# Optimization experiments

Measured on AMD Instinct MI355X. Metric: run time of the kernel, lower is better.

## Reference

```python
import jax, jax.numpy as jnp
import numpy as np

B, S, D = 2, 2048, 4096
NH, NKV = 32, 8
HD = D // NH  # 128
N_REP = NH // NKV  # 4


def setup_inputs() -> dict:
    key = jax.random.key(0)
    ks = jax.random.split(key, 5)
    scale = 0.02
    return {
        "x": jax.random.normal(ks[0], (B, S, D), dtype=jnp.float32),
        "wq": jax.random.normal(ks[1], (D, NH * HD), dtype=jnp.float32) * scale,
        "wk": jax.random.normal(ks[2], (D, NKV * HD), dtype=jnp.float32) * scale,
        "wv": jax.random.normal(ks[3], (D, NKV * HD), dtype=jnp.float32) * scale,
        "wo": jax.random.normal(ks[4], (NH * HD, D), dtype=jnp.float32) * scale,
    }


def reference(x, wq, wk, wv, wo):
    bsz, toks, _ = x.shape
    q = (x @ wq).reshape(bsz, toks, NH, HD)      # [B,S,NH,HD]
    k = (x @ wk).reshape(bsz, toks, NKV, HD)     # [B,S,NKV,HD]
    v = (x @ wv).reshape(bsz, toks, NKV, HD)
    # GQA: fold n_rep into einsum instead of materializing repeated K/V.
    qg = q.reshape(bsz, toks, NKV, N_REP, HD)    # group query heads per kv head
    scores = jnp.einsum('bqgrd,bkgd->bgrqk', qg, k) / jnp.sqrt(jnp.asarray(HD, x.dtype))
    attn = jax.nn.softmax(scores.astype(jnp.float32), axis=-1).astype(x.dtype)
    out = jnp.einsum('bgrqk,bkgd->bqgrd', attn, v)  # [B,S,NKV,N_REP,HD]
    out = out.reshape(bsz, toks, NH * HD)
    return out @ wo
```

## Files before the change

kernel.cpp:

```cpp
#include <hip/hip_runtime.h>
#include <math.h>

typedef _Float16 f16;
using f16x8 = __attribute__((ext_vector_type(8))) _Float16;
using f32x4 = __attribute__((ext_vector_type(4))) float;

#define BATCH 2
#define SEQ   2048
#define DMODEL 4096
#define NH    32
#define NKV   8
#define HD    128
#define MTOK  (BATCH*SEQ)

__global__ __launch_bounds__(256) void cvt_f32_f16_k(const float* __restrict__ in,
                                                     f16* __restrict__ out, int n8) {
  int i = blockIdx.x * 256 + threadIdx.x;
  if (i >= n8) return;
  const float4* p = reinterpret_cast<const float4*>(in) + (size_t)i * 2;
  float4 a = p[0], b = p[1];
  f16x8 o = { (f16)a.x, (f16)a.y, (f16)a.z, (f16)a.w,
              (f16)b.x, (f16)b.y, (f16)b.z, (f16)b.w };
  reinterpret_cast<f16x8*>(out)[i] = o;
}

__global__ __launch_bounds__(256) void transpose_cvt_k(const float* __restrict__ w,
                                                       f16* __restrict__ wt, int Kd, int Nd,
                                                       float scale) {
  __shared__ float tile[32][33];
  const int t = threadIdx.x;
  const int n0 = blockIdx.x * 32, k0 = blockIdx.y * 32;
  const int r = t >> 3, c4 = (t & 7) << 2;
  const float4 v = *reinterpret_cast<const float4*>(w + (size_t)(k0 + r) * Nd + n0 + c4);
  tile[r][c4 + 0] = v.x; tile[r][c4 + 1] = v.y; tile[r][c4 + 2] = v.z; tile[r][c4 + 3] = v.w;
  __syncthreads();
  union { f16 h[4]; ushort4 u4; } pk;
  pk.h[0] = (f16)(tile[c4 + 0][r] * scale);
  pk.h[1] = (f16)(tile[c4 + 1][r] * scale);
  pk.h[2] = (f16)(tile[c4 + 2][r] * scale);
  pk.h[3] = (f16)(tile[c4 + 3][r] * scale);
  *reinterpret_cast<ushort4*>(wt + (size_t)(n0 + r) * Kd + k0 + c4) = pk.u4;
}

template<int MODE>
__global__ __launch_bounds__(256) void gemm_bt_k(const f16* __restrict__ A,
                                                 const f16* __restrict__ BT,
                                                 void* __restrict__ Cv,
                                                 int M, int N, int K) {
  __shared__ f16 Alds[128 * 64];
  __shared__ f16 Blds[128 * 64];
  const int t = threadIdx.x, lane = t & 63, w = t >> 6;
  const int nbn = N >> 7;
  const int nwg = gridDim.x;
  const int cpx = nwg >> 3;
  const int bid = blockIdx.x;
  const int swz = (bid & 7) * cpx + (bid >> 3);
  const int bm = swz / nbn, bn = swz % nbn;
  const size_t m0 = (size_t)bm << 7, n0 = (size_t)bn << 7;

  const int srow = t >> 3;
  const int sslot = t & 7;
  char* ldsAw = (char*)Alds + w * 1024;
  char* ldsBw = (char*)Blds + w * 1024;

  f32x4 acc[4][4];
#pragma unroll
  for (int i = 0; i < 4; i++)
#pragma unroll
    for (int j = 0; j < 4; j++) acc[i][j] = f32x4{0.f, 0.f, 0.f, 0.f};

  const int wr = (w >> 1) << 6, wc = (w & 1) << 6;
  const int ll = lane & 15, lg = lane >> 4;

  for (int kt = 0; kt < K; kt += 64) {
    __syncthreads();
#pragma unroll
    for (int p = 0; p < 4; p++) {
      const int row = srow + (p << 5);
      const int ssrc = (sslot ^ (row & 7)) << 3;
      const f16* gA = A + (m0 + row) * (size_t)K + kt + ssrc;
      __builtin_amdgcn_global_load_lds((const __attribute__((address_space(1))) void*)gA,
          (__attribute__((address_space(3))) void*)(ldsAw + p * 4096), 16, 0, 0);
      const f16* gB = BT + (n0 + row) * (size_t)K + kt + ssrc;
      __builtin_amdgcn_global_load_lds((const __attribute__((address_space(1))) void*)gB,
          (__attribute__((address_space(3))) void*)(ldsBw + p * 4096), 16, 0, 0);
    }
    __syncthreads();
#pragma unroll
    for (int kk = 0; kk < 2; kk++) {
      f16x8 af[4], bfr[4];
      const int slot = (kk << 2) + lg;
#pragma unroll
      for (int i = 0; i < 4; i++) {
        const int r = wr + (i << 4) + ll;
        af[i] = *reinterpret_cast<const f16x8*>((const char*)Alds + r * 128 + ((slot ^ (r & 7)) << 4));
      }
#pragma unroll
      for (int j = 0; j < 4; j++) {
        const int r = wc + (j << 4) + ll;
        bfr[j] = *reinterpret_cast<const f16x8*>((const char*)Blds + r * 128 + ((slot ^ (r & 7)) << 4));
      }
#pragma unroll
      for (int i = 0; i < 4; i++)
#pragma unroll
        for (int j = 0; j < 4; j++)
          acc[i][j] = __builtin_amdgcn_mfma_f32_16x16x32_f16(af[i], bfr[j], acc[i][j], 0, 0, 0);
    }
  }

#pragma unroll
  for (int i = 0; i < 4; i++) {
    const size_t mrow = m0 + wr + (i << 4) + (lg << 2);
#pragma unroll
    for (int j = 0; j < 4; j++) {
      const size_t ncol = n0 + wc + (j << 4) + ll;
      if (MODE == 0) {
        f16* C = (f16*)Cv;
#pragma unroll
        for (int r = 0; r < 4; r++) C[(mrow + r) * N + ncol] = (f16)acc[i][j][r];
      } else if (MODE == 2) {
        float* C = (float*)Cv;
#pragma unroll
        for (int r = 0; r < 4; r++) C[(mrow + r) * N + ncol] = acc[i][j][r];
      } else if (MODE == 3) {
        f16* Kc = (f16*)Cv;
        f16* Vt = (f16*)Cv + (size_t)MTOK * NKV * HD;
        if ((int)ncol < 1024) {
#pragma unroll
          for (int r = 0; r < 4; r++) Kc[(mrow + r) * 1024 + ncol] = (f16)acc[i][j][r];
        } else {
          const int nc = (int)ncol - 1024;
          const int kvh = nc >> 7, d = nc & 127;
          const int b = (int)(mrow >> 11), sc = (int)(mrow & 2047);
          union { f16 h[4]; ushort4 u4; } pk;
#pragma unroll
          for (int r = 0; r < 4; r++) pk.h[r] = (f16)acc[i][j][r];
          *reinterpret_cast<ushort4*>(Vt + (((size_t)(b * NKV + kvh) * HD + d) * SEQ + sc)) = pk.u4;
        }
      }
    }
  }
}

template<int MODE>
__global__ __launch_bounds__(512, 2) void gemm256_k(const f16* __restrict__ A,
                                                    const f16* __restrict__ BT,
                                                    void* __restrict__ Cv,
                                                    int M, int N, int K) {
  __shared__ f16 lds[2 * 4 * 128 * 64];
  char* ldsb = (char*)lds;

  const int t = threadIdx.x, lane = t & 63, w = t >> 6;
  const int wm = w >> 2, wn = w & 3;
  const int ll = lane & 15, lg = lane >> 4;
  const int nbn = N >> 8;
  const int nwg = gridDim.x, cpx = nwg >> 3, bid = blockIdx.x;
  const int swz = (bid & 7) * cpx + (bid >> 3);
  const int bm = swz / nbn, bn = swz % nbn;
  const size_t m0 = (size_t)bm << 8, n0 = (size_t)bn << 8;
  const int NT = K >> 6;

  auto stage = [&](int bufI, int unit, int ktS) {
    const f16* base = (unit < 2) ? (A + (m0 + (size_t)(unit & 1) * 128) * (size_t)K)
                                 : (BT + (n0 + (size_t)(unit & 1) * 128) * (size_t)K);
#pragma unroll
    for (int rr = 0; rr < 2; rr++) {
      const int u = t + rr * 512;
      const int row = u >> 3, lin = u & 7;
      const int slot = lin ^ (row & 7);
      const f16* src = base + (size_t)row * K + ktS + slot * 8;
      char* dst = ldsb + (size_t)(bufI * 4 + unit) * 16384 + (size_t)(w * 64 + rr * 512) * 16;
      __builtin_amdgcn_global_load_lds((const __attribute__((address_space(1))) void*)src,
          (__attribute__((address_space(3))) void*)dst, 16, 0, 0);
    }
  };

  f32x4 acc[8][4];
#pragma unroll
  for (int i = 0; i < 8; i++)
#pragma unroll
    for (int j = 0; j < 4; j++) acc[i][j] = f32x4{0.f, 0.f, 0.f, 0.f};

  f16x8 af[4][2];
  f16x8 bfr[2][2][2];

  stage(0, 0, 0); stage(0, 2, 0); stage(0, 3, 0); stage(0, 1, 0);
  stage(1, 0, 64); stage(1, 2, 64); stage(1, 3, 64);
  asm volatile("s_waitcnt vmcnt(6)" ::: "memory");
  __builtin_amdgcn_sched_barrier(0);
  __builtin_amdgcn_s_barrier();

#define PH(RBUF, RDA, RDB, SBUF, SUNIT, STILE, VM, MH, NHQ) do {                          \
    if ((RDA) >= 0) {                                                                     \
      const char* ab = ldsb + (size_t)((RBUF) * 4 + (RDA)) * 16384;                       \
      _Pragma("unroll") for (int mi = 0; mi < 4; mi++)                                    \
        _Pragma("unroll") for (int kk = 0; kk < 2; kk++)                                  \
          af[mi][kk] = *reinterpret_cast<const f16x8*>(ab + (mi * 32 + wm * 16 + ll) * 128\
                               + ((((kk << 2) + lg) ^ (ll & 7)) << 4));                   \
    }                                                                                     \
    if ((RDB) >= 0) {                                                                     \
      const char* bb = ldsb + (size_t)((RBUF) * 4 + 2 + (RDB)) * 16384;                   \
      _Pragma("unroll") for (int ni = 0; ni < 2; ni++)                                    \
        _Pragma("unroll") for (int kk = 0; kk < 2; kk++)                                  \
          bfr[RDB][ni][kk] = *reinterpret_cast<const f16x8*>(bb +                         \
                               (wn * 32 + ni * 16 + ll) * 128                             \
                               + ((((kk << 2) + lg) ^ (ll & 7)) << 4));                   \
    }                                                                                     \
    stage((SBUF), (SUNIT), ((STILE) & (NT - 1)) << 6);                                    \
    if (VM) { asm volatile("s_waitcnt vmcnt(6)" ::: "memory");                            \
              __builtin_amdgcn_sched_barrier(0); }                                        \
    __builtin_amdgcn_s_barrier();                                                         \
    asm volatile("s_waitcnt lgkmcnt(0)" ::: "memory");                                    \
    __builtin_amdgcn_sched_barrier(0);                                                    \
    __builtin_amdgcn_s_setprio(1);                                                        \
    _Pragma("unroll") for (int kk = 0; kk < 2; kk++)                                      \
      _Pragma("unroll") for (int mi = 0; mi < 4; mi++)                                    \
        _Pragma("unroll") for (int ni = 0; ni < 2; ni++)                                  \
          acc[(MH) * 4 + mi][(NHQ) * 2 + ni] = __builtin_amdgcn_mfma_f32_16x16x32_f16(    \
              af[mi][kk], bfr[NHQ][ni][kk], acc[(MH) * 4 + mi][(NHQ) * 2 + ni], 0, 0, 0); \
    __builtin_amdgcn_s_setprio(0);                                                        \
    __builtin_amdgcn_s_barrier();                                                         \
  } while (0)

  for (int tt = 0; tt < NT; tt += 2) {
    PH(0,  0,  0, 1, 1, tt + 1, false, 0, 0);
    PH(0, -1,  1, 0, 0, tt + 2, false, 0, 1);
    PH(0,  1, -1, 0, 2, tt + 2, false, 1, 0);
    PH(0, -1, -1, 0, 3, tt + 2, true , 1, 1);
    PH(1,  0,  0, 0, 1, tt + 2, false, 0, 0);
    PH(1, -1,  1, 1, 0, tt + 3, false, 0, 1);
    PH(1,  1, -1, 1, 2, tt + 3, false, 1, 0);
    PH(1, -1, -1, 1, 3, tt + 3, true , 1, 1);
  }
#undef PH

#pragma unroll
  for (int mh = 0; mh < 2; mh++)
#pragma unroll
    for (int mi = 0; mi < 4; mi++) {
      const size_t r0 = m0 + mh * 128 + mi * 32 + wm * 16 + lg * 4;
#pragma unroll
      for (int nh = 0; nh < 2; nh++)
#pragma unroll
        for (int ni = 0; ni < 2; ni++) {
          const size_t c = n0 + nh * 128 + wn * 32 + ni * 16 + ll;
          const f32x4 v = acc[mh * 4 + mi][nh * 2 + ni];
          if (MODE == 0) {
            f16* C = (f16*)Cv;
#pragma unroll
            for (int rr = 0; rr < 4; rr++) C[(r0 + rr) * N + c] = (f16)v[rr];
          } else {
            float* C = (float*)Cv;
#pragma unroll
            for (int rr = 0; rr < 4; rr++) C[(r0 + rr) * N + c] = v[rr];
          }
        }
    }
}

__global__ __launch_bounds__(512) void attn_k7(const f16* __restrict__ Q,
                                               const f16* __restrict__ Kb,
                                               const f16* __restrict__ VT,
                                               f16* __restrict__ ctx) {
  __shared__ f16 Klds[2][64 * 128];
  __shared__ f16 Vlds[2][128 * 64];
  __shared__ f16 Plds[8][16 * 64];

  const int t = threadIdx.x, lane = t & 63, w = t >> 6;
  const int bid = blockIdx.x;
  const int swz = (bid & 7) * 128 + (bid >> 3);
  const int qt = swz & 63, kvh = (swz >> 6) & 7, b = swz >> 9;
  const int h = kvh * 4 + (w & 3);
  const int q0 = qt * 32 + (w >> 2) * 16;
  const int ll = lane & 15, lg = lane >> 4;

  const f16* Qb = Q + ((size_t)(b * SEQ + q0) * NH + h) * HD;
  const f16* Kh = Kb + ((size_t)b * SEQ * NKV + kvh) * HD;
  const f16* Vh = VT + ((size_t)(b * NKV + kvh)) * HD * SEQ;

  f16x8 qf[4];
#pragma unroll
  for (int kd = 0; kd < 4; kd++)
    qf[kd] = *reinterpret_cast<const f16x8*>(Qb + (size_t)ll * (NH * HD) + kd * 32 + lg * 8);

  float m_ = -INFINITY;
  float l_ = 0.f;
  f32x4 o[8];
#pragma unroll
  for (int df = 0; df < 8; df++) o[df] = f32x4{0.f, 0.f, 0.f, 0.f};

  const float THR = 11.5416f;

  auto stage = [&](int bufi, int kt) {
#pragma unroll
    for (int rr = 0; rr < 2; rr++) {
      const int u = w * 128 + rr * 64 + lane;
      const int krow = u >> 4, klin = u & 15;
      const int kslot = klin ^ (krow & 7);
      const f16* ksrc = Kh + (size_t)(kt + krow) * (NKV * HD) + kslot * 8;
      __builtin_amdgcn_global_load_lds((const __attribute__((address_space(1))) void*)ksrc,
          (__attribute__((address_space(3))) void*)((char*)&Klds[bufi][0] + (size_t)u * 16), 16, 0, 0);
      const int vrow = u >> 3, vlin = u & 7;
      const int vslot = vlin ^ (vrow & 7);
      const f16* vsrc = Vh + (size_t)vrow * SEQ + kt + vslot * 8;
      __builtin_amdgcn_global_load_lds((const __attribute__((address_space(1))) void*)vsrc,
          (__attribute__((address_space(3))) void*)((char*)&Vlds[bufi][0] + (size_t)u * 16), 16, 0, 0);
    }
  };

  stage(0, 0);
  __syncthreads();

  for (int kt = 0; kt < SEQ; kt += 64) {
    const int buf = (kt >> 6) & 1;
    if (kt + 64 < SEQ) stage(buf ^ 1, kt + 64);

    const char* Kt = (const char*)Klds[buf];
    const char* Vt = (const char*)Vlds[buf];

    f32x4 s[4];
#pragma unroll
    for (int nf = 0; nf < 4; nf++) {
      f32x4 a = f32x4{0.f, 0.f, 0.f, 0.f};
#pragma unroll
      for (int kd = 0; kd < 4; kd++) {
        const int row = nf * 16 + ll;
        f16x8 kf = *reinterpret_cast<const f16x8*>(
            Kt + row * 256 + ((((kd << 2) + lg) ^ (row & 7)) << 4));
        a = __builtin_amdgcn_mfma_f32_16x16x32_f16(kf, qf[kd], a, 0, 0, 0);
      }
      s[nf] = a;
    }

    float mx = s[0][0];
#pragma unroll
    for (int nf = 0; nf < 4; nf++)
#pragma unroll
      for (int r = 0; r < 4; r++) mx = fmaxf(mx, s[nf][r]);

    if (!__all((int)(mx <= m_ + THR))) {
      float mr = fmaxf(mx, __shfl_xor(mx, 16, 64));
      mr = fmaxf(mr, __shfl_xor(mr, 32, 64));
      const float mn = fmaxf(m_, mr);
      const float corrq = __builtin_amdgcn_exp2f(m_ - mn);
      m_ = mn;
      l_ *= corrq;
#pragma unroll
      for (int r = 0; r < 4; r++) {
        const float c = __shfl(corrq, (lane & 48) | (lg * 4 + r), 64);
#pragma unroll
        for (int df = 0; df < 8; df++) o[df][r] *= c;
      }
    }

    float rs = 0.f;
#pragma unroll
    for (int nf = 0; nf < 4; nf++)
#pragma unroll
      for (int r = 0; r < 4; r++) {
        const float p = __builtin_amdgcn_exp2f(s[nf][r] - m_);
        s[nf][r] = p;
        rs += p;
      }
    rs += __shfl_xor(rs, 16, 64);
    rs += __shfl_xor(rs, 32, 64);
    l_ += rs;

    char* Pw = (char*)&Plds[w][0];
#pragma unroll
    for (int nf = 0; nf < 4; nf++) {
      union { f16 h[4]; ushort4 u4; } pk;
#pragma unroll
      for (int r = 0; r < 4; r++) pk.h[r] = (f16)s[nf][r];
      *reinterpret_cast<ushort4*>(Pw + ll * 128 + ((nf * 32 + lg * 8) ^ ((ll & 7) << 4))) = pk.u4;
    }

    f16x8 pf[2];
#pragma unroll
    for (int kf = 0; kf < 2; kf++)
      pf[kf] = *reinterpret_cast<const f16x8*>(Pw + ll * 128 + (((kf << 6) + (lg << 4)) ^ ((ll & 7) << 4)));

#pragma unroll
    for (int kf = 0; kf < 2; kf++)
#pragma unroll
      for (int df = 0; df < 8; df++) {
        const int row = df * 16 + ll;
        f16x8 vf = *reinterpret_cast<const f16x8*>(
            Vt + row * 128 + ((((kf << 2) + lg) ^ (row & 7)) << 4));
        o[df] = __builtin_amdgcn_mfma_f32_16x16x32_f16(pf[kf], vf, o[df], 0, 0, 0);
      }

    __syncthreads();
  }

  float inv[4];
#pragma unroll
  for (int r = 0; r < 4; r++) {
    const float lq = __shfl(l_, (lane & 48) | (lg * 4 + r), 64);
    inv[r] = 1.0f / lq;
  }
  f16* cb = ctx + ((size_t)(b * SEQ + q0) * NH + h) * HD;
#pragma unroll
  for (int df = 0; df < 8; df++)
#pragma unroll
    for (int r = 0; r < 4; r++)
      cb[(size_t)(lg * 4 + r) * (NH * HD) + df * 16 + ll] = (f16)(o[df][r] * inv[r]);
}

extern "C" void kernel_launch(void* const* d_in, const int* in_sizes, int n_in,
                              void* d_out, int out_size, void* d_ws, size_t ws_size,
                              hipStream_t stream) {
  (void)in_sizes; (void)n_in; (void)out_size;
  const float* x  = (const float*)d_in[0];
  const float* wq = (const float*)d_in[1];
  const float* wk = (const float*)d_in[2];
  const float* wv = (const float*)d_in[3];
  const float* wo = (const float*)d_in[4];
  float* out = (float*)d_out;

  const size_t SZ_X  = (size_t)MTOK * DMODEL * sizeof(f16);
  const size_t SZ_KV = (size_t)MTOK * NKV * HD * sizeof(f16);
  if (ws_size < 3 * SZ_X + 2 * SZ_KV) return;

  char* ws = (char*)d_ws;
  f16* xh  = (f16*)ws;
  f16* wT  = (f16*)(ws + SZ_X);
  f16* Qb  = (f16*)(ws + 2 * SZ_X);
  f16* Kb  = (f16*)(ws + 3 * SZ_X);
  f16* VTb = (f16*)(ws + 3 * SZ_X + SZ_KV);

  const float KSC2 = 0.08838834764831845f * 1.4426950408889634f;

  cvt_f32_f16_k<<<dim3(MTOK * DMODEL / 8 / 256), 256, 0, stream>>>(x, xh, MTOK * DMODEL / 8);

  transpose_cvt_k<<<dim3(DMODEL / 32, DMODEL / 32), 256, 0, stream>>>(wq, wT, DMODEL, DMODEL, KSC2);
  gemm256_k<0><<<dim3((MTOK / 256) * (DMODEL / 256)), 512, 0, stream>>>(xh, wT, Qb, MTOK, DMODEL, DMODEL);

  transpose_cvt_k<<<dim3(NKV * HD / 32, DMODEL / 32), 256, 0, stream>>>(wk, wT, DMODEL, NKV * HD, 1.0f);
  transpose_cvt_k<<<dim3(NKV * HD / 32, DMODEL / 32), 256, 0, stream>>>(wv, wT + (size_t)1024 * DMODEL, DMODEL, NKV * HD, 1.0f);
  gemm_bt_k<3><<<dim3((MTOK / 128) * (2048 / 128)), 256, 0, stream>>>(xh, wT, Kb, MTOK, 2048, DMODEL);

  attn_k7<<<dim3(BATCH * NKV * (SEQ / 32)), 512, 0, stream>>>(Qb, Kb, VTb, xh);

  transpose_cvt_k<<<dim3(DMODEL / 32, DMODEL / 32), 256, 0, stream>>>(wo, wT, DMODEL, DMODEL, 1.0f);
  gemm256_k<2><<<dim3((MTOK / 256) * (DMODEL / 256)), 512, 0, stream>>>(xh, wT, out, MTOK, DMODEL, DMODEL);
}
```

Measured before the change: 551.4 us.

## Process two 16-row query tiles per wave in attention and merge K/V weight transposes

The attention kernel now has each wave handle 32 query rows, as two 16-row halves, against each staged K/V tile. This doubles the reuse of every K and V tile loaded into LDS and halves the number of workgroups and global K/V loads. In exchange each wave holds twice as many accumulator and Q registers, and the launch bound asks for 2 blocks per CU, which risks register pressure or spills. The two separate wk/wv transpose launches are also merged into one launch that uses a z grid dimension.

```diff
diff --git a/kernel.cpp b/kernel.cpp
--- a/kernel.cpp
+++ b/kernel.cpp
@@ -40,6 +40,26 @@
   pk.h[2] = (f16)(tile[c4 + 2][r] * scale);
   pk.h[3] = (f16)(tile[c4 + 3][r] * scale);
   *reinterpret_cast<ushort4*>(wt + (size_t)(n0 + r) * Kd + k0 + c4) = pk.u4;
+}
+
+__global__ __launch_bounds__(256) void transpose_cvt2_k(const float* __restrict__ w0,
+                                                        const float* __restrict__ w1,
+                                                        f16* __restrict__ wt, int Kd, int Nd) {
+  __shared__ float tile[32][33];
+  const float* w = blockIdx.z ? w1 : w0;
+  f16* dst = wt + (size_t)blockIdx.z * Nd * Kd;
+  const int t = threadIdx.x;
+  const int n0 = blockIdx.x * 32, k0 = blockIdx.y * 32;
+  const int r = t >> 3, c4 = (t & 7) << 2;
+  const float4 v = *reinterpret_cast<const float4*>(w + (size_t)(k0 + r) * Nd + n0 + c4);
+  tile[r][c4 + 0] = v.x; tile[r][c4 + 1] = v.y; tile[r][c4 + 2] = v.z; tile[r][c4 + 3] = v.w;
+  __syncthreads();
+  union { f16 h[4]; ushort4 u4; } pk;
+  pk.h[0] = (f16)tile[c4 + 0][r];
+  pk.h[1] = (f16)tile[c4 + 1][r];
+  pk.h[2] = (f16)tile[c4 + 2][r];
+  pk.h[3] = (f16)tile[c4 + 3][r];
+  *reinterpret_cast<ushort4*>(dst + (size_t)(n0 + r) * Kd + k0 + c4) = pk.u4;
 }
 
 template<int MODE>
@@ -258,36 +278,37 @@
     }
 }
 
-__global__ __launch_bounds__(512) void attn_k7(const f16* __restrict__ Q,
-                                               const f16* __restrict__ Kb,
-                                               const f16* __restrict__ VT,
-                                               f16* __restrict__ ctx) {
+__global__ __launch_bounds__(512, 2) void attn_k8(const f16* __restrict__ Q,
+                                                  const f16* __restrict__ Kb,
+                                                  const f16* __restrict__ VT,
+                                                  f16* __restrict__ ctx) {
   __shared__ f16 Klds[2][64 * 128];
   __shared__ f16 Vlds[2][128 * 64];
   __shared__ f16 Plds[8][16 * 64];
 
   const int t = threadIdx.x, lane = t & 63, w = t >> 6;
   const int bid = blockIdx.x;
-  const int swz = (bid & 7) * 128 + (bid >> 3);
-  const int qt = swz & 63, kvh = (swz >> 6) & 7, b = swz >> 9;
+  const int swz = (bid & 7) * 64 + (bid >> 3);
+  const int qt = swz & 31, kvh = (swz >> 5) & 7, b = swz >> 8;
   const int h = kvh * 4 + (w & 3);
-  const int q0 = qt * 32 + (w >> 2) * 16;
+  const int q0 = qt * 64 + (w >> 2) * 32;
   const int ll = lane & 15, lg = lane >> 4;
 
   const f16* Qb = Q + ((size_t)(b * SEQ + q0) * NH + h) * HD;
   const f16* Kh = Kb + ((size_t)b * SEQ * NKV + kvh) * HD;
   const f16* Vh = VT + ((size_t)(b * NKV + kvh)) * HD * SEQ;
 
-  f16x8 qf[4];
-#pragma unroll
-  for (int kd = 0; kd < 4; kd++)
-    qf[kd] = *reinterpret_cast<const f16x8*>(Qb + (size_t)ll * (NH * HD) + kd * 32 + lg * 8);
-
-  float m_ = -INFINITY;
-  float l_ = 0.f;
-  f32x4 o[8];
-#pragma unroll
-  for (int df = 0; df < 8; df++) o[df] = f32x4{0.f, 0.f, 0.f, 0.f};
+  f16x8 qf0[4], qf1[4];
+#pragma unroll
+  for (int kd = 0; kd < 4; kd++) {
+    qf0[kd] = *reinterpret_cast<const f16x8*>(Qb + (size_t)ll * (NH * HD) + kd * 32 + lg * 8);
+    qf1[kd] = *reinterpret_cast<const f16x8*>(Qb + (size_t)(16 + ll) * (NH * HD) + kd * 32 + lg * 8);
+  }
+
+  float m0_ = -INFINITY, l0_ = 0.f, m1_ = -INFINITY, l1_ = 0.f;
+  f32x4 o0[8], o1[8];
+#pragma unroll
+  for (int df = 0; df < 8; df++) { o0[df] = f32x4{0.f, 0.f, 0.f, 0.f}; o1[df] = f32x4{0.f, 0.f, 0.f, 0.f}; }
 
   const float THR = 11.5416f;
 
@@ -308,16 +329,7 @@
     }
   };
 
-  stage(0, 0);
-  __syncthreads();
-
-  for (int kt = 0; kt < SEQ; kt += 64) {
-    const int buf = (kt >> 6) & 1;
-    if (kt + 64 < SEQ) stage(buf ^ 1, kt + 64);
-
-    const char* Kt = (const char*)Klds[buf];
-    const char* Vt = (const char*)Vlds[buf];
-
+  auto half = [&](const char* Kt, const f16x8* qf, float& m_, float& l_, f32x4* o, f16x8* pf) {
     f32x4 s[4];
 #pragma unroll
     for (int nf = 0; nf < 4; nf++) {
@@ -374,11 +386,24 @@
       for (int r = 0; r < 4; r++) pk.h[r] = (f16)s[nf][r];
       *reinterpret_cast<ushort4*>(Pw + ll * 128 + ((nf * 32 + lg * 8) ^ ((ll & 7) << 4))) = pk.u4;
     }
-
-    f16x8 pf[2];
 #pragma unroll
     for (int kf = 0; kf < 2; kf++)
       pf[kf] = *reinterpret_cast<const f16x8*>(Pw + ll * 128 + (((kf << 6) + (lg << 4)) ^ ((ll & 7) << 4)));
+  };
+
+  stage(0, 0);
+  __syncthreads();
+
+  for (int kt = 0; kt < SEQ; kt += 64) {
+    const int buf = (kt >> 6) & 1;
+    if (kt + 64 < SEQ) stage(buf ^ 1, kt + 64);
+
+    const char* Kt = (const char*)Klds[buf];
+    const char* Vt = (const char*)Vlds[buf];
+
+    f16x8 pf0[2], pf1[2];
+    half(Kt, qf0, m0_, l0_, o0, pf0);
+    half(Kt, qf1, m1_, l1_, o1, pf1);
 
 #pragma unroll
     for (int kf = 0; kf < 2; kf++)
@@ -387,24 +412,28 @@
         const int row = df * 16 + ll;
         f16x8 vf = *reinterpret_cast<const f16x8*>(
             Vt + row * 128 + ((((kf << 2) + lg) ^ (row & 7)) << 4));
-        o[df] = __builtin_amdgcn_mfma_f32_16x16x32_f16(pf[kf], vf, o[df], 0, 0, 0);
+        o0[df] = __builtin_amdgcn_mfma_f32_16x16x32_f16(pf0[kf], vf, o0[df], 0, 0, 0);
+        o1[df] = __builtin_amdgcn_mfma_f32_16x16x32_f16(pf1[kf], vf, o1[df], 0, 0, 0);
       }
 
     __syncthreads();
   }
 
-  float inv[4];
+  float inv0[4], inv1[4];
 #pragma unroll
   for (int r = 0; r < 4; r++) {
-    const float lq = __shfl(l_, (lane & 48) | (lg * 4 + r), 64);
-    inv[r] = 1.0f / lq;
-  }
-  f16* cb = ctx + ((size_t)(b * SEQ + q0) * NH + h) * HD;
+    inv0[r] = 1.0f / __shfl(l0_, (lane & 48) | (lg * 4 + r), 64);
+    inv1[r] = 1.0f / __shfl(l1_, (lane & 48) | (lg * 4 + r), 64);
+  }
+  f16* cb0 = ctx + ((size_t)(b * SEQ + q0) * NH + h) * HD;
+  f16* cb1 = ctx + ((size_t)(b * SEQ + q0 + 16) * NH + h) * HD;
 #pragma unroll
   for (int df = 0; df < 8; df++)
 #pragma unroll
-    for (int r = 0; r < 4; r++)
-      cb[(size_t)(lg * 4 + r) * (NH * HD) + df * 16 + ll] = (f16)(o[df][r] * inv[r]);
+    for (int r = 0; r < 4; r++) {
+      cb0[(size_t)(lg * 4 + r) * (NH * HD) + df * 16 + ll] = (f16)(o0[df][r] * inv0[r]);
+      cb1[(size_t)(lg * 4 + r) * (NH * HD) + df * 16 + ll] = (f16)(o1[df][r] * inv1[r]);
+    }
 }
 
 extern "C" void kernel_launch(void* const* d_in, const int* in_sizes, int n_in,
@@ -436,11 +465,10 @@
   transpose_cvt_k<<<dim3(DMODEL / 32, DMODEL / 32), 256, 0, stream>>>(wq, wT, DMODEL, DMODEL, KSC2);
   gemm256_k<0><<<dim3((MTOK / 256) * (DMODEL / 256)), 512, 0, stream>>>(xh, wT, Qb, MTOK, DMODEL, DMODEL);
 
-  transpose_cvt_k<<<dim3(NKV * HD / 32, DMODEL / 32), 256, 0, stream>>>(wk, wT, DMODEL, NKV * HD, 1.0f);
-  transpose_cvt_k<<<dim3(NKV * HD / 32, DMODEL / 32), 256, 0, stream>>>(wv, wT + (size_t)1024 * DMODEL, DMODEL, NKV * HD, 1.0f);
+  transpose_cvt2_k<<<dim3(NKV * HD / 32, DMODEL / 32, 2), 256, 0, stream>>>(wk, wv, wT, DMODEL, NKV * HD);
   gemm_bt_k<3><<<dim3((MTOK / 128) * (2048 / 128)), 256, 0, stream>>>(xh, wT, Kb, MTOK, 2048, DMODEL);
 
-  attn_k7<<<dim3(BATCH * NKV * (SEQ / 32)), 512, 0, stream>>>(Qb, Kb, VTb, xh);
+  attn_k8<<<dim3(BATCH * NKV * (SEQ / 64)), 512, 0, stream>>>(Qb, Kb, VTb, xh);
 
   transpose_cvt_k<<<dim3(DMODEL / 32, DMODEL / 32), 256, 0, stream>>>(wo, wT, DMODEL, DMODEL, 1.0f);
   gemm256_k<2><<<dim3((MTOK / 256) * (DMODEL / 256)), 512, 0, stream>>>(xh, wT, out, MTOK, DMODEL, DMODEL);
```

Result: no change. 553.7 us (+0.4%).

## Replace KV projection GEMM with pipelined 128x256 double-buffered kernel, merge transposes

Applied to the files above, without the earlier changes.

Swaps the simple single-buffered 128x128 K/V projection GEMM for a 512-thread 128x256 tile kernel. It stages A and B sub-tiles into double-buffered LDS with global_load_lds, interleaves loads with MFMA phases, and uses explicit waitcnt, barriers and setprio. The two weight transpose launches for wk and wv are merged into one launch over a z dimension. The aim is to hide global-load latency behind compute and cut launch overhead, at the cost of more LDS per block and tight hand-tuned synchronisation.

```diff
diff --git a/kernel.cpp b/kernel.cpp
--- a/kernel.cpp
+++ b/kernel.cpp
@@ -42,26 +42,68 @@
   *reinterpret_cast<ushort4*>(wt + (size_t)(n0 + r) * Kd + k0 + c4) = pk.u4;
 }
 
-template<int MODE>
-__global__ __launch_bounds__(256) void gemm_bt_k(const f16* __restrict__ A,
-                                                 const f16* __restrict__ BT,
-                                                 void* __restrict__ Cv,
-                                                 int M, int N, int K) {
-  __shared__ f16 Alds[128 * 64];
-  __shared__ f16 Blds[128 * 64];
+__global__ __launch_bounds__(256) void transpose_cvt2_k(const float* __restrict__ w0,
+                                                        const float* __restrict__ w1,
+                                                        f16* __restrict__ wt, int Kd, int Nd) {
+  __shared__ float tile[32][33];
+  const float* w = blockIdx.z ? w1 : w0;
+  f16* dst = wt + (size_t)blockIdx.z * Nd * Kd;
+  const int t = threadIdx.x;
+  const int n0 = blockIdx.x * 32, k0 = blockIdx.y * 32;
+  const int r = t >> 3, c4 = (t & 7) << 2;
+  const float4 v = *reinterpret_cast<const float4*>(w + (size_t)(k0 + r) * Nd + n0 + c4);
+  tile[r][c4 + 0] = v.x; tile[r][c4 + 1] = v.y; tile[r][c4 + 2] = v.z; tile[r][c4 + 3] = v.w;
+  __syncthreads();
+  union { f16 h[4]; ushort4 u4; } pk;
+  pk.h[0] = (f16)tile[c4 + 0][r];
+  pk.h[1] = (f16)tile[c4 + 1][r];
+  pk.h[2] = (f16)tile[c4 + 2][r];
+  pk.h[3] = (f16)tile[c4 + 3][r];
+  *reinterpret_cast<ushort4*>(dst + (size_t)(n0 + r) * Kd + k0 + c4) = pk.u4;
+}
+
+__global__ __launch_bounds__(512, 2) void gemm_kv8_k(const f16* __restrict__ A,
+                                                     const f16* __restrict__ BT,
+                                                     f16* __restrict__ Kc,
+                                                     f16* __restrict__ Vt,
+                                                     int M, int N, int K) {
+  __shared__ f16 lds[2 * 24576];
+  char* ldsb = (char*)lds;
+
   const int t = threadIdx.x, lane = t & 63, w = t >> 6;
-  const int nbn = N >> 7;
-  const int nwg = gridDim.x;
-  const int cpx = nwg >> 3;
-  const int bid = blockIdx.x;
+  const int wm = w >> 2, wn = w & 3;
+  const int ll = lane & 15, lg = lane >> 4;
+  const int nbn = N >> 8;
+  const int nwg = gridDim.x, cpx = nwg >> 3, bid = blockIdx.x;
   const int swz = (bid & 7) * cpx + (bid >> 3);
   const int bm = swz / nbn, bn = swz % nbn;
-  const size_t m0 = (size_t)bm << 7, n0 = (size_t)bn << 7;
-
-  const int srow = t >> 3;
-  const int sslot = t & 7;
-  char* ldsAw = (char*)Alds + w * 1024;
-  char* ldsBw = (char*)Blds + w * 1024;
+  const size_t m0 = (size_t)bm << 7, n0 = (size_t)bn << 8;
+  const int NT = K >> 6;
+
+  const int uoff[4] = {0, 8192, 16384, 32768};
+
+  auto stage = [&](int bufI, int unit, int ktS) {
+    char* dstb = ldsb + (size_t)bufI * 49152 + uoff[unit];
+    if (unit < 2) {
+      const f16* base = A + (m0 + (size_t)(unit & 1) * 64) * (size_t)K;
+      const int row = t >> 3, lin = t & 7;
+      const int slot = lin ^ (row & 7);
+      const f16* src = base + (size_t)row * K + ktS + slot * 8;
+      __builtin_amdgcn_global_load_lds((const __attribute__((address_space(1))) void*)src,
+          (__attribute__((address_space(3))) void*)(dstb + (size_t)t * 16), 16, 0, 0);
+    } else {
+      const f16* base = BT + (n0 + (size_t)(unit & 1) * 128) * (size_t)K;
+#pragma unroll
+      for (int rr = 0; rr < 2; rr++) {
+        const int u = t + rr * 512;
+        const int row = u >> 3, lin = u & 7;
+        const int slot = lin ^ (row & 7);
+        const f16* src = base + (size_t)row * K + ktS + slot * 8;
+        __builtin_amdgcn_global_load_lds((const __attribute__((address_space(1))) void*)src,
+            (__attribute__((address_space(3))) void*)(dstb + (size_t)u * 16), 16, 0, 0);
+      }
+    }
+  };
 
   f32x4 acc[4][4];
 #pragma unroll
@@ -69,77 +111,88 @@
 #pragma unroll
     for (int j = 0; j < 4; j++) acc[i][j] = f32x4{0.f, 0.f, 0.f, 0.f};
 
-  const int wr = (w >> 1) << 6, wc = (w & 1) << 6;
-  const int ll = lane & 15, lg = lane >> 4;
-
-  for (int kt = 0; kt < K; kt += 64) {
-    __syncthreads();
-#pragma unroll
-    for (int p = 0; p < 4; p++) {
-      const int row = srow + (p << 5);
-      const int ssrc = (sslot ^ (row & 7)) << 3;
-      const f16* gA = A + (m0 + row) * (size_t)K + kt + ssrc;
-      __builtin_amdgcn_global_load_lds((const __attribute__((address_space(1))) void*)gA,
-          (__attribute__((address_space(3))) void*)(ldsAw + p * 4096), 16, 0, 0);
-      const f16* gB = BT + (n0 + row) * (size_t)K + kt + ssrc;
-      __builtin_amdgcn_global_load_lds((const __attribute__((address_space(1))) void*)gB,
-          (__attribute__((address_space(3))) void*)(ldsBw + p * 4096), 16, 0, 0);
-    }
-    __syncthreads();
-#pragma unroll
-    for (int kk = 0; kk < 2; kk++) {
-      f16x8 af[4], bfr[4];
-      const int slot = (kk << 2) + lg;
-#pragma unroll
-      for (int i = 0; i < 4; i++) {
-        const int r = wr + (i << 4) + ll;
-        af[i] = *reinterpret_cast<const f16x8*>((const char*)Alds + r * 128 + ((slot ^ (r & 7)) << 4));
-      }
-#pragma unroll
-      for (int j = 0; j < 4; j++) {
-        const int r = wc + (j << 4) + ll;
-        bfr[j] = *reinterpret_cast<const f16x8*>((const char*)Blds + r * 128 + ((slot ^ (r & 7)) << 4));
-      }
-#pragma unroll
-      for (int i = 0; i < 4; i++)
-#pragma unroll
-        for (int j = 0; j < 4; j++)
-          acc[i][j] = __builtin_amdgcn_mfma_f32_16x16x32_f16(af[i], bfr[j], acc[i][j], 0, 0, 0);
-    }
+  f16x8 af[2][2];
+  f16x8 bfr[2][2][2];
+
+  stage(0, 0, 0); stage(0, 1, 0); stage(0, 2, 0); stage(0, 3, 0);
+  stage(1, 0, 64); stage(1, 2, 64); stage(1, 3, 64);
+  asm volatile("s_waitcnt vmcnt(5)" ::: "memory");
+  __builtin_amdgcn_sched_barrier(0);
+  __builtin_amdgcn_s_barrier();
+
+#define PHK(RBUF, RDA, RDB, SBUF, SUNIT, STILE, VM, MH, NHQ) do {                         \
+    if ((RDA) >= 0) {                                                                     \
+      const char* ab = ldsb + (size_t)(RBUF) * 49152 + uoff[MH];                          \
+      _Pragma("unroll") for (int mi2 = 0; mi2 < 2; mi2++)                                 \
+        _Pragma("unroll") for (int kk = 0; kk < 2; kk++) {                                \
+          const int ri = wm * 32 + mi2 * 16 + ll;                                         \
+          af[mi2][kk] = *reinterpret_cast<const f16x8*>(ab + ri * 128                     \
+                               + ((((kk << 2) + lg) ^ (ri & 7)) << 4));                   \
+        }                                                                                 \
+    }                                                                                     \
+    if ((RDB) >= 0) {                                                                     \
+      const char* bb = ldsb + (size_t)(RBUF) * 49152 + uoff[2 + (RDB)];                   \
+      _Pragma("unroll") for (int ni2 = 0; ni2 < 2; ni2++)                                 \
+        _Pragma("unroll") for (int kk = 0; kk < 2; kk++) {                                \
+          const int ri = wn * 32 + ni2 * 16 + ll;                                         \
+          bfr[RDB][ni2][kk] = *reinterpret_cast<const f16x8*>(bb + ri * 128               \
+                               + ((((kk << 2) + lg) ^ (ri & 7)) << 4));                   \
+        }                                                                                 \
+    }                                                                                     \
+    stage((SBUF), (SUNIT), ((STILE) & (NT - 1)) << 6);                                    \
+    if (VM) { asm volatile("s_waitcnt vmcnt(5)" ::: "memory");                            \
+              __builtin_amdgcn_sched_barrier(0); }                                        \
+    __builtin_amdgcn_s_barrier();                                                         \
+    asm volatile("s_waitcnt lgkmcnt(0)" ::: "memory");                                    \
+    __builtin_amdgcn_sched_barrier(0);                                                    \
+    __builtin_amdgcn_s_setprio(1);                                                        \
+    _Pragma("unroll") for (int kk = 0; kk < 2; kk++)                                      \
+      _Pragma("unroll") for (int mi2 = 0; mi2 < 2; mi2++)                                 \
+        _Pragma("unroll") for (int ni2 = 0; ni2 < 2; ni2++)                               \
+          acc[(MH) * 2 + mi2][(NHQ) * 2 + ni2] = __builtin_amdgcn_mfma_f32_16x16x32_f16(  \
+              af[mi2][kk], bfr[NHQ][ni2][kk], acc[(MH) * 2 + mi2][(NHQ) * 2 + ni2],       \
+              0, 0, 0);                                                                   \
+    __builtin_amdgcn_s_setprio(0);                                                        \
+    __builtin_amdgcn_s_barrier();                                                         \
+  } while (0)
+
+  for (int tt = 0; tt < NT; tt += 2) {
+    PHK(0,  0,  0, 1, 1, tt + 1, false, 0, 0);
+    PHK(0, -1,  1, 0, 0, tt + 2, false, 0, 1);
+    PHK(0,  1, -1, 0, 2, tt + 2, false, 1, 0);
+    PHK(0, -1, -1, 0, 3, tt + 2, true , 1, 1);
+    PHK(1,  0,  0, 0, 1, tt + 2, false, 0, 0);
+    PHK(1, -1,  1, 1, 0, tt + 3, false, 0, 1);
+    PHK(1,  1, -1, 1, 2, tt + 3, false, 1, 0);
+    PHK(1, -1, -1, 1, 3, tt + 3, true , 1, 1);
   }
-
-#pragma unroll
-  for (int i = 0; i < 4; i++) {
-    const size_t mrow = m0 + wr + (i << 4) + (lg << 2);
-#pragma unroll
-    for (int j = 0; j < 4; j++) {
-      const size_t ncol = n0 + wc + (j << 4) + ll;
-      if (MODE == 0) {
-        f16* C = (f16*)Cv;
-#pragma unroll
-        for (int r = 0; r < 4; r++) C[(mrow + r) * N + ncol] = (f16)acc[i][j][r];
-      } else if (MODE == 2) {
-        float* C = (float*)Cv;
-#pragma unroll
-        for (int r = 0; r < 4; r++) C[(mrow + r) * N + ncol] = acc[i][j][r];
-      } else if (MODE == 3) {
-        f16* Kc = (f16*)Cv;
-        f16* Vt = (f16*)Cv + (size_t)MTOK * NKV * HD;
-        if ((int)ncol < 1024) {
-#pragma unroll
-          for (int r = 0; r < 4; r++) Kc[(mrow + r) * 1024 + ncol] = (f16)acc[i][j][r];
-        } else {
-          const int nc = (int)ncol - 1024;
-          const int kvh = nc >> 7, d = nc & 127;
-          const int b = (int)(mrow >> 11), sc = (int)(mrow & 2047);
-          union { f16 h[4]; ushort4 u4; } pk;
-#pragma unroll
-          for (int r = 0; r < 4; r++) pk.h[r] = (f16)acc[i][j][r];
-          *reinterpret_cast<ushort4*>(Vt + (((size_t)(b * NKV + kvh) * HD + d) * SEQ + sc)) = pk.u4;
+#undef PHK
+
+#pragma unroll
+  for (int mh = 0; mh < 2; mh++)
+#pragma unroll
+    for (int mi2 = 0; mi2 < 2; mi2++) {
+      const size_t r0 = m0 + mh * 64 + wm * 32 + mi2 * 16 + lg * 4;
+#pragma unroll
+      for (int nh = 0; nh < 2; nh++)
+#pragma unroll
+        for (int ni2 = 0; ni2 < 2; ni2++) {
+          const size_t c = n0 + nh * 128 + wn * 32 + ni2 * 16 + ll;
+          const f32x4 v = acc[mh * 2 + mi2][nh * 2 + ni2];
+          if ((int)c < 1024) {
+#pragma unroll
+            for (int rr = 0; rr < 4; rr++) Kc[(r0 + rr) * 1024 + c] = (f16)v[rr];
+          } else {
+            const int nc = (int)c - 1024;
+            const int kvh = nc >> 7, d = nc & 127;
+            const int b = (int)(r0 >> 11), sc = (int)(r0 & 2047);
+            union { f16 h[4]; ushort4 u4; } pk;
+#pragma unroll
+            for (int rr = 0; rr < 4; rr++) pk.h[rr] = (f16)v[rr];
+            *reinterpret_cast<ushort4*>(Vt + (((size_t)(b * NKV + kvh) * HD + d) * SEQ + sc)) = pk.u4;
+          }
         }
-      }
-    }
-  }
+    }
 }
 
 template<int MODE>
@@ -258,7 +311,7 @@
     }
 }
 
-__global__ __launch_bounds__(512) void attn_k7(const f16* __restrict__ Q,
+__global__ __launch_bounds__(512) void attn_k9(const f16* __restrict__ Q,
                                                const f16* __restrict__ Kb,
                                                const f16* __restrict__ VT,
                                                f16* __restrict__ ctx) {
@@ -436,11 +489,10 @@
   transpose_cvt_k<<<dim3(DMODEL / 32, DMODEL / 32), 256, 0, stream>>>(wq, wT, DMODEL, DMODEL, KSC2);
   gemm256_k<0><<<dim3((MTOK / 256) * (DMODEL / 256)), 512, 0, stream>>>(xh, wT, Qb, MTOK, DMODEL, DMODEL);
 
-  transpose_cvt_k<<<dim3(NKV * HD / 32, DMODEL / 32), 256, 0, stream>>>(wk, wT, DMODEL, NKV * HD, 1.0f);
-  transpose_cvt_k<<<dim3(NKV * HD / 32, DMODEL / 32), 256, 0, stream>>>(wv, wT + (size_t)1024 * DMODEL, DMODEL, NKV * HD, 1.0f);
-  gemm_bt_k<3><<<dim3((MTOK / 128) * (2048 / 128)), 256, 0, stream>>>(xh, wT, Kb, MTOK, 2048, DMODEL);
-
-  attn_k7<<<dim3(BATCH * NKV * (SEQ / 32)), 512, 0, stream>>>(Qb, Kb, VTb, xh);
+  transpose_cvt2_k<<<dim3(NKV * HD / 32, DMODEL / 32, 2), 256, 0, stream>>>(wk, wv, wT, DMODEL, NKV * HD);
+  gemm_kv8_k<<<dim3((MTOK / 128) * (2048 / 256)), 512, 0, stream>>>(xh, wT, Kb, VTb, MTOK, 2048, DMODEL);
+
+  attn_k9<<<dim3(BATCH * NKV * (SEQ / 32)), 512, 0, stream>>>(Qb, Kb, VTb, xh);
 
   transpose_cvt_k<<<dim3(DMODEL / 32, DMODEL / 32), 256, 0, stream>>>(wo, wT, DMODEL, DMODEL, 1.0f);
   gemm256_k<2><<<dim3((MTOK / 256) * (DMODEL / 256)), 512, 0, stream>>>(xh, wT, out, MTOK, DMODEL, DMODEL);
```

Result: faster. 535.4 us (-2.9%).
